# Optimization experiments

Hardware: AMD Instinct MI355X
Metric: run time of the kernel (lower is better)

The kernel has to match this reference:

```python
import jax, jax.numpy as jnp
import numpy as np

BETA = 0.5
TAU_L = 0.1
TAU_H = 0.1
TOP_K = 2


def setup_inputs() -> dict:
    key = jax.random.key(0)
    ks = jax.random.split(key, 6)
    B, S, H, F, E, NH = 1, 2048, 1024, 3584, 8, 16
    hidden_states = jax.random.normal(ks[0], (B, S, H), dtype=jnp.float32)
    self_attn_weights = jax.random.uniform(ks[1], (B, NH, S, S), dtype=jnp.float32)
    gate_w = jax.random.normal(ks[2], (E, H), dtype=jnp.float32) * 0.02
    w1 = jax.random.normal(ks[3], (E, F, H), dtype=jnp.float32) * 0.02
    w2 = jax.random.normal(ks[4], (E, H, F), dtype=jnp.float32) * 0.02
    w3 = jax.random.normal(ks[5], (E, F, H), dtype=jnp.float32) * 0.02
    return {"hidden_states": hidden_states, "self_attn_weights": self_attn_weights,
            "gate_w": gate_w, "w1": w1, "w2": w2, "w3": w3}


def reference(hidden_states, self_attn_weights, gate_w, w1, w2, w3):
    B, S, H = hidden_states.shape
    E = gate_w.shape[0]
    x = hidden_states.reshape(-1, H)          # [T, H], T = B*S
    T = x.shape[0]

    router_logits = x @ gate_w.T              # [T, E]
    rw_full = jax.nn.softmax(router_logits.astype(jnp.float32), axis=-1)
    rw, sel = jax.lax.top_k(rw_full, TOP_K)   # [T, 2]

    # --- dynamic pruning branch (loss_index < block_range) ---
    mask_top1 = rw[:, 1] < BETA * rw[:, 0]
    new_routing = jnp.ones_like(rw)
    new_routing = new_routing.at[:, 1].set(jnp.where(mask_top1, 0.0, 1.0))

    # sequence_length > 1: attention-based token pruning (assumes B == 1)
    mean_tensor = jnp.mean(jnp.squeeze(self_attn_weights), axis=0)  # [S, S]
    column = mean_tensor.shape[1]
    real_number = jnp.arange(column, 0, -1, dtype=jnp.float32)
    attention_scores = jnp.sum(mean_tensor, axis=1) / real_number   # [S]
    l1_norm = jnp.sum(jnp.abs(x), axis=1)                           # [T]
    attention_scores = attention_scores * l1_norm

    n_low = int(TAU_L * T)
    n_high = int(TAU_H * T)
    _, low_idx = jax.lax.top_k(-attention_scores, n_low)   # smallest
    _, high_idx = jax.lax.top_k(attention_scores, n_high)  # largest
    mask_all = jnp.zeros((T,), dtype=bool).at[low_idx].set(True)
    keep_all = jnp.zeros((T,), dtype=bool).at[high_idx].set(True)
    new_routing = jnp.where(mask_all[:, None], 0.0, new_routing)
    new_routing = jnp.where(keep_all[:, None], 1.0, new_routing)

    rw = rw * new_routing
    denom = jnp.sum(rw, axis=-1, keepdims=True)
    rw = rw / jnp.where(denom > 0, denom, 1.0)  # fully-masked tokens -> 0 output
    rw = rw.astype(x.dtype)

    # combine weights per (token, expert); dispatch mask == new_routing
    cw = jnp.sum(rw[:, :, None] * jax.nn.one_hot(sel, E, dtype=rw.dtype), axis=1)  # [T, E]

    # dense reference for the gather-expert-scatter loop (SwiGLU experts)
    h = jnp.einsum('th,efh->tef', x, w1)      # [T, E, F]
    g = jnp.einsum('th,efh->tef', x, w3)
    a = jax.nn.silu(h) * g
    y = jnp.einsum('tef,ehf->teh', a, w2)     # [T, E, H]
    out = jnp.einsum('te,teh->th', cw, y)     # [T, H]

    return out.reshape(B, S, H), router_logits
```

## Files before the change

kernel.cpp:

```cpp
#include <hip/hip_runtime.h>
#include <hip/hip_bf16.h>
#include <math.h>

#define NTOK 2048
#define HDIM 1024
#define NEXP 8
#define FDIM 3584
#define NHEADS 16
#define NLOW 204
#define NHIGH 204
#define BK 64
#define KSPLIT 4
#define KCH (FDIM / KSPLIT)

typedef __bf16 bf16x8 __attribute__((ext_vector_type(8)));
typedef float f32x4 __attribute__((ext_vector_type(4)));

__device__ __forceinline__ void gload16(__hip_bfloat16* lds, const __hip_bfloat16* g)
{
    __builtin_amdgcn_global_load_lds(
        (const __attribute__((address_space(1))) unsigned int*)g,
        (__attribute__((address_space(3))) unsigned int*)lds, 16, 0, 0);
}

__device__ __forceinline__ void cvt8(const float* __restrict__ s,
                                     __hip_bfloat16* __restrict__ d)
{
    float4 a = *(const float4*)s;
    float4 b = *(const float4*)(s + 4);
    bf16x8 v;
    v[0] = (__bf16)a.x; v[1] = (__bf16)a.y; v[2] = (__bf16)a.z; v[3] = (__bf16)a.w;
    v[4] = (__bf16)b.x; v[5] = (__bf16)b.y; v[6] = (__bf16)b.z; v[7] = (__bf16)b.w;
    *(bf16x8*)d = v;
}

#define NZ   (NTOK * HDIM / 4)
#define NX   (NTOK * HDIM / 8)
#define NWT  (NEXP * FDIM * HDIM / 8)
__global__ __launch_bounds__(256) void k_prep(
    const float* __restrict__ x, const float* __restrict__ w1,
    const float* __restrict__ w3, float4* __restrict__ outz,
    __hip_bfloat16* __restrict__ xb, __hip_bfloat16* __restrict__ wb1,
    __hip_bfloat16* __restrict__ wb3)
{
    size_t gid = (size_t)blockIdx.x * 256 + threadIdx.x;
    size_t stride = (size_t)gridDim.x * 256;
    size_t total = (size_t)NZ + NX + 2 * (size_t)NWT;
    for (size_t i = gid; i < total; i += stride) {
        if (i < NZ) {
            outz[i] = make_float4(0.f, 0.f, 0.f, 0.f);
        } else if (i < (size_t)NZ + NX) {
            size_t j = (i - NZ) * 8;
            cvt8(x + j, xb + j);
        } else if (i < (size_t)NZ + NX + NWT) {
            size_t j = (i - NZ - NX) * 8;
            cvt8(w1 + j, wb1 + j);
        } else {
            size_t j = (i - NZ - NX - NWT) * 8;
            cvt8(w3 + j, wb3 + j);
        }
    }
}

__global__ __launch_bounds__(256) void k_router(
    const float* __restrict__ x, const float* __restrict__ gw,
    float* __restrict__ logits, float* __restrict__ l1,
    int* __restrict__ sel0, int* __restrict__ sel1,
    float* __restrict__ rw0, float* __restrict__ rw1)
{
    __shared__ float sgw[NEXP * HDIM];
    int tid = threadIdx.x;
    for (int i = tid; i < NEXP * HDIM; i += 256) sgw[i] = gw[i];
    __syncthreads();
    int wv = tid >> 6, lane = tid & 63;
    int t = blockIdx.x * 4 + wv;
    const float* xr = x + (size_t)t * HDIM;
    float acc[NEXP];
#pragma unroll
    for (int e = 0; e < NEXP; ++e) acc[e] = 0.f;
    float al1 = 0.f;
    for (int h = lane; h < HDIM; h += 64) {
        float xv = xr[h];
        al1 += fabsf(xv);
#pragma unroll
        for (int e = 0; e < NEXP; ++e) acc[e] += xv * sgw[e * HDIM + h];
    }
#pragma unroll
    for (int off = 32; off > 0; off >>= 1) {
#pragma unroll
        for (int e = 0; e < NEXP; ++e) acc[e] += __shfl_xor(acc[e], off);
        al1 += __shfl_xor(al1, off);
    }
    if (lane < NEXP) logits[t * NEXP + lane] = acc[lane];
    if (lane == 0) {
        l1[t] = al1;
        float m = acc[0];
#pragma unroll
        for (int e = 1; e < NEXP; ++e) m = fmaxf(m, acc[e]);
        float p[NEXP], s = 0.f;
#pragma unroll
        for (int e = 0; e < NEXP; ++e) { p[e] = expf(acc[e] - m); s += p[e]; }
        float inv = 1.f / s;
        float b0 = -1.f, b1 = -1.f; int i0 = 0, i1 = 0;
#pragma unroll
        for (int e = 0; e < NEXP; ++e) {
            float r = p[e] * inv;
            if (r > b0) { b1 = b0; i1 = i0; b0 = r; i0 = e; }
            else if (r > b1) { b1 = r; i1 = e; }
        }
        sel0[t] = i0; sel1[t] = i1; rw0[t] = b0; rw1[t] = b1;
    }
}

__global__ __launch_bounds__(256) void k_attn(
    const float* __restrict__ attn, const float* __restrict__ l1,
    float* __restrict__ scores)
{
    int i = blockIdx.x, tid = threadIdx.x;
    float acc = 0.f;
    for (int h = 0; h < NHEADS; ++h) {
        const float4* p = (const float4*)(attn + ((size_t)h * NTOK + i) * NTOK);
        for (int j = tid; j < NTOK / 4; j += 256) {
            float4 v = p[j];
            acc += v.x + v.y + v.z + v.w;
        }
    }
    __shared__ float red[256];
    red[tid] = acc; __syncthreads();
    for (int s = 128; s > 0; s >>= 1) {
        if (tid < s) red[tid] += red[tid + s];
        __syncthreads();
    }
    if (tid == 0) scores[i] = red[0] / (16.f * (float)(NTOK - i)) * l1[i];
}

__global__ __launch_bounds__(256) void k_rank(
    const float* __restrict__ scores, const float* __restrict__ rw0,
    const float* __restrict__ rw1, float* __restrict__ w0f, float* __restrict__ w1f)
{
    __shared__ float s[NTOK];
    int tid = threadIdx.x;
    for (int i = tid; i < NTOK; i += 256) s[i] = scores[i];
    __syncthreads();
    int t = blockIdx.x * 256 + tid;
    float st = s[t];
    int cl = 0, ch = 0;
    for (int j = 0; j < NTOK; ++j) {
        float sj = s[j];
        int tie = (sj == st) && (j < t);
        cl += (sj < st) || tie;
        ch += (sj > st) || tie;
    }
    bool in_low = cl < NLOW, keep = ch < NHIGH;
    float a = rw0[t], b = rw1[t];
    float n0 = 1.f, n1 = (b < 0.5f * a) ? 0.f : 1.f;
    if (in_low) { n0 = 0.f; n1 = 0.f; }
    if (keep)   { n0 = 1.f; n1 = 1.f; }
    a *= n0; b *= n1;
    float d = a + b;
    if (d > 0.f) { a /= d; b /= d; }
    w0f[t] = a; w1f[t] = b;
}

__global__ __launch_bounds__(512) void k_build(
    const int* __restrict__ sel0, const int* __restrict__ sel1,
    const float* __restrict__ w0f, const float* __restrict__ w1f,
    int* __restrict__ tok, float* __restrict__ wgt,
    int* __restrict__ counts, int* __restrict__ offs)
{
    int tid = threadIdx.x;
    int e = tid >> 6, lane = tid & 63;
    unsigned long long below = (1ull << lane) - 1ull;
    int base = 0;
    for (int r = 0; r < NTOK / 64; ++r) {
        int t = r * 64 + lane;
        bool f0 = (sel0[t] == e) && (w0f[t] > 0.f);
        unsigned long long m0 = __ballot(f0);
        if (f0) {
            int pos = base + __popcll(m0 & below);
            tok[e * NTOK + pos] = t; wgt[e * NTOK + pos] = w0f[t];
        }
        base += __popcll(m0);
        bool f1 = (sel1[t] == e) && (w1f[t] > 0.f);
        unsigned long long m1 = __ballot(f1);
        if (f1) {
            int pos = base + __popcll(m1 & below);
            tok[e * NTOK + pos] = t; wgt[e * NTOK + pos] = w1f[t];
        }
        base += __popcll(m1);
    }
    if (lane == 0) counts[e] = base;
    __syncthreads();
    if (tid == 0) {
        int o = 0;
        for (int i = 0; i < NEXP; ++i) { offs[i] = o; o += counts[i]; }
    }
}

__global__ __launch_bounds__(256, 3) void k_ffn1(
    const __hip_bfloat16* __restrict__ xb, const __hip_bfloat16* __restrict__ wb1,
    const __hip_bfloat16* __restrict__ wb3,
    const float* __restrict__ w2, __hip_bfloat16* __restrict__ wb2,
    const int* __restrict__ tok, const float* __restrict__ wgt,
    const int* __restrict__ counts, const int* __restrict__ offs,
    __hip_bfloat16* __restrict__ act)
{
    int tid = threadIdx.x;
    if (blockIdx.z == 0) {
        size_t gid = ((size_t)(blockIdx.y * gridDim.x + blockIdx.x) * 256 + tid);
        size_t stride = (size_t)gridDim.x * gridDim.y * 256;
        for (size_t i = gid; i < (size_t)NWT; i += stride)
            cvt8(w2 + i * 8, wb2 + i * 8);
        return;
    }
    int e = blockIdx.z - 1;
    int cnt = counts[e];
    int m0 = blockIdx.y * 128;
    if (m0 >= cnt) return;
    int f0 = blockIdx.x * 64;
    __shared__ __align__(16) __hip_bfloat16 sX[128 * BK];
    __shared__ __align__(16) __hip_bfloat16 sW1[64 * BK];
    __shared__ __align__(16) __hip_bfloat16 sW3[64 * BK];
    __shared__ int sTok[128];
    __shared__ float sWgt[128];
    if (tid < 128) {
        int row = m0 + tid;
        int rr = (row < cnt) ? row : (cnt - 1);
        sTok[tid] = tok[e * NTOK + rr];
        sWgt[tid] = (row < cnt) ? wgt[e * NTOK + row] : 0.f;
    }
    __syncthreads();

    int wv = tid >> 6, lane = tid & 63;
    int lr = lane >> 3;
    int sw8 = (((lane & 7) ^ lr) << 3);

    const __hip_bfloat16* gx[4];
    __hip_bfloat16* lx[4];
#pragma unroll
    for (int j = 0; j < 4; ++j) {
        int c = 4 * wv + j;
        gx[j] = xb + (size_t)sTok[8 * c + lr] * HDIM + sw8;
        lx[j] = sX + c * 512;
    }
    const __hip_bfloat16* gw1[2]; const __hip_bfloat16* gw3[2];
    __hip_bfloat16* lw1[2]; __hip_bfloat16* lw3[2];
#pragma unroll
    for (int j = 0; j < 2; ++j) {
        int c = 2 * wv + j;
        gw1[j] = wb1 + ((size_t)e * FDIM + f0 + 8 * c + lr) * HDIM + sw8;
        gw3[j] = wb3 + ((size_t)e * FDIM + f0 + 8 * c + lr) * HDIM + sw8;
        lw1[j] = sW1 + c * 512;
        lw3[j] = sW3 + c * 512;
    }

    int colx = lane & 15;
    int swz = (colx & 7) << 4;
    int kb0 = (lane >> 4) * 16;
    f32x4 acc1[2][4] = {}, acc3[2][4] = {};

    for (int k0 = 0; k0 < HDIM; k0 += BK) {
#pragma unroll
        for (int j = 0; j < 4; ++j) gload16(lx[j], gx[j] + k0);
#pragma unroll
        for (int j = 0; j < 2; ++j) {
            gload16(lw1[j], gw1[j] + k0);
            gload16(lw3[j], gw3[j] + k0);
        }
        __syncthreads();
#pragma unroll
        for (int ks = 0; ks < 2; ++ks) {
            int off = ((kb0 + ks * 64) ^ swz) >> 1;
            bf16x8 a_[2];
#pragma unroll
            for (int m = 0; m < 2; ++m) {
                int row = 32 * wv + m * 16 + colx;
                a_[m] = *(const bf16x8*)&sX[(row << 6) + off];
            }
#pragma unroll
            for (int f = 0; f < 4; ++f) {
                int row = f * 16 + colx;
                bf16x8 b1 = *(const bf16x8*)&sW1[(row << 6) + off];
                bf16x8 b3 = *(const bf16x8*)&sW3[(row << 6) + off];
#pragma unroll
                for (int m = 0; m < 2; ++m) {
                    acc1[m][f] = __builtin_amdgcn_mfma_f32_16x16x32_bf16(a_[m], b1, acc1[m][f], 0, 0, 0);
                    acc3[m][f] = __builtin_amdgcn_mfma_f32_16x16x32_bf16(a_[m], b3, acc3[m][f], 0, 0, 0);
                }
            }
        }
        __syncthreads();
    }
    int soff = offs[e];
    int lane4 = (lane >> 4) * 4;
#pragma unroll
    for (int m = 0; m < 2; ++m) {
        int rbase = 32 * wv + m * 16 + lane4;
#pragma unroll
        for (int q = 0; q < 4; ++q) {
            int rloc = rbase + q;
            if (m0 + rloc < cnt) {
                float wgtv = sWgt[rloc];
#pragma unroll
                for (int f = 0; f < 4; ++f) {
                    float hv = acc1[m][f][q], gv = acc3[m][f][q];
                    float av = hv / (1.f + expf(-hv)) * gv * wgtv;
                    act[(size_t)(soff + m0 + rloc) * FDIM + f0 + f * 16 + colx] =
                        (__hip_bfloat16)av;
                }
            }
        }
    }
}

__global__ __launch_bounds__(256, 4) void k_ffn2(
    const __hip_bfloat16* __restrict__ act, const __hip_bfloat16* __restrict__ wb2,
    const int* __restrict__ tok, const int* __restrict__ counts,
    const int* __restrict__ offs, float* __restrict__ out)
{
    int z = blockIdx.z;
    int e = z >> 2;
    int kbase = (z & 3) * KCH;
    int cnt = counts[e];
    int m0 = blockIdx.y * 128;
    if (m0 >= cnt) return;
    int h0 = blockIdx.x * 64;
    int tid = threadIdx.x;
    __shared__ __align__(16) __hip_bfloat16 sA[128 * BK];
    __shared__ __align__(16) __hip_bfloat16 sB[64 * BK];
    __shared__ int sTok[128];
    if (tid < 128) {
        int row = m0 + tid;
        sTok[tid] = (row < cnt) ? tok[e * NTOK + row] : 0;
    }
    __syncthreads();
    int soff = offs[e];
    int wv = tid >> 6, lane = tid & 63;
    int lr = lane >> 3;
    int sw8 = (((lane & 7) ^ lr) << 3);

    const __hip_bfloat16* ga[4];
    __hip_bfloat16* la[4];
#pragma unroll
    for (int j = 0; j < 4; ++j) {
        int c = 4 * wv + j;
        int trow = 8 * c + lr;
        int arow = (m0 + trow < cnt) ? (m0 + trow) : (cnt - 1);
        ga[j] = act + (size_t)(soff + arow) * FDIM + kbase + sw8;
        la[j] = sA + c * 512;
    }
    const __hip_bfloat16* gb[2];
    __hip_bfloat16* lb[2];
#pragma unroll
    for (int j = 0; j < 2; ++j) {
        int c = 2 * wv + j;
        gb[j] = wb2 + ((size_t)e * HDIM + h0 + 8 * c + lr) * FDIM + kbase + sw8;
        lb[j] = sB + c * 512;
    }

    int colx = lane & 15;
    int swz = (colx & 7) << 4;
    int kb0 = (lane >> 4) * 16;
    f32x4 acc[2][4] = {};

    for (int k0 = 0; k0 < KCH; k0 += BK) {
#pragma unroll
        for (int j = 0; j < 4; ++j) gload16(la[j], ga[j] + k0);
#pragma unroll
        for (int j = 0; j < 2; ++j) gload16(lb[j], gb[j] + k0);
        __syncthreads();
#pragma unroll
        for (int ks = 0; ks < 2; ++ks) {
            int off = ((kb0 + ks * 64) ^ swz) >> 1;
            bf16x8 a_[2];
#pragma unroll
            for (int m = 0; m < 2; ++m) {
                int row = 32 * wv + m * 16 + colx;
                a_[m] = *(const bf16x8*)&sA[(row << 6) + off];
            }
#pragma unroll
            for (int f = 0; f < 4; ++f) {
                int row = f * 16 + colx;
                bf16x8 b = *(const bf16x8*)&sB[(row << 6) + off];
#pragma unroll
                for (int m = 0; m < 2; ++m)
                    acc[m][f] = __builtin_amdgcn_mfma_f32_16x16x32_bf16(a_[m], b, acc[m][f], 0, 0, 0);
            }
        }
        __syncthreads();
    }
    int lane4 = (lane >> 4) * 4;
#pragma unroll
    for (int m = 0; m < 2; ++m) {
        int rbase = 32 * wv + m * 16 + lane4;
#pragma unroll
        for (int q = 0; q < 4; ++q) {
            int rloc = rbase + q;
            if (m0 + rloc < cnt) {
                int t = sTok[rloc];
#pragma unroll
                for (int f = 0; f < 4; ++f)
                    atomicAdd(&out[(size_t)t * HDIM + h0 + f * 16 + colx], acc[m][f][q]);
            }
        }
    }
}

extern "C" void kernel_launch(void* const* d_in, const int* in_sizes, int n_in,
                              void* d_out, int out_size, void* d_ws, size_t ws_size,
                              hipStream_t stream)
{
    const float* x    = (const float*)d_in[0];
    const float* attn = (const float*)d_in[1];
    const float* gw   = (const float*)d_in[2];
    const float* w1   = (const float*)d_in[3];
    const float* w2   = (const float*)d_in[4];
    const float* w3   = (const float*)d_in[5];
    float* out = (float*)d_out;
    float* logits = out + (size_t)NTOK * HDIM;

    char* ws = (char*)d_ws;
    float* l1     = (float*)(ws + 0);
    float* scores = (float*)(ws + 8192);
    int*   sel0   = (int*)(ws + 16384);
    int*   sel1   = (int*)(ws + 24576);
    float* rw0    = (float*)(ws + 32768);
    float* rw1    = (float*)(ws + 40960);
    float* w0f    = (float*)(ws + 49152);
    float* w1f    = (float*)(ws + 57344);
    int*   counts = (int*)(ws + 65536);
    int*   offs   = (int*)(ws + 65600);
    int*   tok    = (int*)(ws + 73728);
    float* wgt    = (float*)(ws + 143360);
    __hip_bfloat16* act = (__hip_bfloat16*)(ws + 1048576);
    __hip_bfloat16* xb  = (__hip_bfloat16*)(ws + 33554432);
    __hip_bfloat16* wb1 = (__hip_bfloat16*)(ws + 67108864);
    __hip_bfloat16* wb3 = (__hip_bfloat16*)(ws + 134217728);
    __hip_bfloat16* wb2 = (__hip_bfloat16*)(ws + 201326592);

    k_prep<<<4096, 256, 0, stream>>>(x, w1, w3, (float4*)out, xb, wb1, wb3);
    k_router<<<NTOK / 4, 256, 0, stream>>>(x, gw, logits, l1, sel0, sel1, rw0, rw1);
    k_attn<<<NTOK, 256, 0, stream>>>(attn, l1, scores);
    k_rank<<<NTOK / 256, 256, 0, stream>>>(scores, rw0, rw1, w0f, w1f);
    k_build<<<1, 512, 0, stream>>>(sel0, sel1, w0f, w1f, tok, wgt, counts, offs);
    k_ffn1<<<dim3(FDIM / 64, NTOK / 128, NEXP + 1), 256, 0, stream>>>(
        xb, wb1, wb3, w2, wb2, tok, wgt, counts, offs, act);
    k_ffn2<<<dim3(HDIM / 64, NTOK / 128, NEXP * KSPLIT), 256, 0, stream>>>(
        act, wb2, tok, counts, offs, out);
}
```

Before: 407.2 us.

## Fuse attention row-sum into prep kernel and raise ffn2 split-K to 8

Merges the attention-score reduction into the front conversion kernel as extra blocks, so the two memory-bound passes share one launch and can overlap. The l1 scaling moves into the ranking kernel. It also doubles the K-split for the second expert GEMM to increase block-level parallelism, at the cost of more atomic accumulations into the output.

```diff
diff --git a/kernel.cpp b/kernel.cpp
--- a/kernel.cpp
+++ b/kernel.cpp
@@ -10,7 +10,7 @@
 #define NLOW 204
 #define NHIGH 204
 #define BK 64
-#define KSPLIT 4
+#define KSPLIT 8
 #define KCH (FDIM / KSPLIT)
 
 typedef __bf16 bf16x8 __attribute__((ext_vector_type(8)));
@@ -37,14 +37,36 @@
 #define NZ   (NTOK * HDIM / 4)
 #define NX   (NTOK * HDIM / 8)
 #define NWT  (NEXP * FDIM * HDIM / 8)
-__global__ __launch_bounds__(256) void k_prep(
-    const float* __restrict__ x, const float* __restrict__ w1,
-    const float* __restrict__ w3, float4* __restrict__ outz,
+
+__global__ __launch_bounds__(256) void k_front(
+    const float* __restrict__ attn, const float* __restrict__ x,
+    const float* __restrict__ w1, const float* __restrict__ w3,
+    float* __restrict__ rawsum, float4* __restrict__ outz,
     __hip_bfloat16* __restrict__ xb, __hip_bfloat16* __restrict__ wb1,
     __hip_bfloat16* __restrict__ wb3)
 {
-    size_t gid = (size_t)blockIdx.x * 256 + threadIdx.x;
-    size_t stride = (size_t)gridDim.x * 256;
+    __shared__ float red[256];
+    int bid = blockIdx.x, tid = threadIdx.x;
+    if (bid < NTOK) {
+        int i = bid;
+        float acc = 0.f;
+        for (int h = 0; h < NHEADS; ++h) {
+            const float4* p = (const float4*)(attn + ((size_t)h * NTOK + i) * NTOK);
+            for (int j = tid; j < NTOK / 4; j += 256) {
+                float4 v = p[j];
+                acc += v.x + v.y + v.z + v.w;
+            }
+        }
+        red[tid] = acc; __syncthreads();
+        for (int s = 128; s > 0; s >>= 1) {
+            if (tid < s) red[tid] += red[tid + s];
+            __syncthreads();
+        }
+        if (tid == 0) rawsum[i] = red[0];
+        return;
+    }
+    size_t gid = (size_t)(bid - NTOK) * 256 + tid;
+    size_t stride = (size_t)(gridDim.x - NTOK) * 256;
     size_t total = (size_t)NZ + NX + 2 * (size_t)NWT;
     for (size_t i = gid; i < total; i += stride) {
         if (i < NZ) {
@@ -112,35 +134,15 @@
     }
 }
 
-__global__ __launch_bounds__(256) void k_attn(
-    const float* __restrict__ attn, const float* __restrict__ l1,
-    float* __restrict__ scores)
-{
-    int i = blockIdx.x, tid = threadIdx.x;
-    float acc = 0.f;
-    for (int h = 0; h < NHEADS; ++h) {
-        const float4* p = (const float4*)(attn + ((size_t)h * NTOK + i) * NTOK);
-        for (int j = tid; j < NTOK / 4; j += 256) {
-            float4 v = p[j];
-            acc += v.x + v.y + v.z + v.w;
-        }
-    }
-    __shared__ float red[256];
-    red[tid] = acc; __syncthreads();
-    for (int s = 128; s > 0; s >>= 1) {
-        if (tid < s) red[tid] += red[tid + s];
-        __syncthreads();
-    }
-    if (tid == 0) scores[i] = red[0] / (16.f * (float)(NTOK - i)) * l1[i];
-}
-
 __global__ __launch_bounds__(256) void k_rank(
-    const float* __restrict__ scores, const float* __restrict__ rw0,
-    const float* __restrict__ rw1, float* __restrict__ w0f, float* __restrict__ w1f)
+    const float* __restrict__ rawsum, const float* __restrict__ l1,
+    const float* __restrict__ rw0, const float* __restrict__ rw1,
+    float* __restrict__ w0f, float* __restrict__ w1f)
 {
     __shared__ float s[NTOK];
     int tid = threadIdx.x;
-    for (int i = tid; i < NTOK; i += 256) s[i] = scores[i];
+    for (int i = tid; i < NTOK; i += 256)
+        s[i] = rawsum[i] / (16.f * (float)(NTOK - i)) * l1[i];
     __syncthreads();
     int t = blockIdx.x * 256 + tid;
     float st = s[t];
@@ -319,8 +321,8 @@
     const int* __restrict__ offs, float* __restrict__ out)
 {
     int z = blockIdx.z;
-    int e = z >> 2;
-    int kbase = (z & 3) * KCH;
+    int e = z >> 3;
+    int kbase = (z & 7) * KCH;
     int cnt = counts[e];
     int m0 = blockIdx.y * 128;
     if (m0 >= cnt) return;
@@ -421,7 +423,7 @@
 
     char* ws = (char*)d_ws;
     float* l1     = (float*)(ws + 0);
-    float* scores = (float*)(ws + 8192);
+    float* rawsum = (float*)(ws + 8192);
     int*   sel0   = (int*)(ws + 16384);
     int*   sel1   = (int*)(ws + 24576);
     float* rw0    = (float*)(ws + 32768);
@@ -438,10 +440,10 @@
     __hip_bfloat16* wb3 = (__hip_bfloat16*)(ws + 134217728);
     __hip_bfloat16* wb2 = (__hip_bfloat16*)(ws + 201326592);
 
-    k_prep<<<4096, 256, 0, stream>>>(x, w1, w3, (float4*)out, xb, wb1, wb3);
+    k_front<<<4096, 256, 0, stream>>>(attn, x, w1, w3, rawsum, (float4*)out,
+                                      xb, wb1, wb3);
     k_router<<<NTOK / 4, 256, 0, stream>>>(x, gw, logits, l1, sel0, sel1, rw0, rw1);
-    k_attn<<<NTOK, 256, 0, stream>>>(attn, l1, scores);
-    k_rank<<<NTOK / 256, 256, 0, stream>>>(scores, rw0, rw1, w0f, w1f);
+    k_rank<<<NTOK / 256, 256, 0, stream>>>(rawsum, l1, rw0, rw1, w0f, w1f);
     k_build<<<1, 512, 0, stream>>>(sel0, sel1, w0f, w1f, tok, wgt, counts, offs);
     k_ffn1<<<dim3(FDIM / 64, NTOK / 128, NEXP + 1), 256, 0, stream>>>(
         xb, wb1, wb3, w2, wb2, tok, wgt, counts, offs, act);
```

Result: slower. 433.6 us (+6.5%).

## Fuse fp32-to-bf16 conversion of w1/w3 into register-prefetched double-buffered FFN1 GEMM

Applied to the files above, without the earlier changes.

The separate pre-pass that converted w1 and w3 from fp32 to bf16 in global memory is removed. k_ffn1 now loads fp32 weights directly, converts them in registers, and stores them into double-buffered padded LDS tiles, prefetching the next K slice during the MFMAs. The F tile grows to 128 with a 64x64 per-wave output and BK drops to 32. This avoids writing and re-reading bf16 weight copies, but each token tile re-reads fp32 weights (twice the bytes per load), and the larger accumulator set raises register pressure, so occupancy is lowered to 2.

```diff
diff --git a/kernel.cpp b/kernel.cpp
--- a/kernel.cpp
+++ b/kernel.cpp
@@ -9,7 +9,9 @@
 #define NHEADS 16
 #define NLOW 204
 #define NHIGH 204
-#define BK 64
+#define BK1 32
+#define LDST 40
+#define BK2 64
 #define KSPLIT 4
 #define KCH (FDIM / KSPLIT)
 
@@ -34,30 +36,43 @@
     *(bf16x8*)d = v;
 }
 
+struct F16v { float4 a, b, c, d; };
+__device__ __forceinline__ F16v ld16(const float* __restrict__ p)
+{
+    F16v v;
+    v.a = *(const float4*)p;
+    v.b = *(const float4*)(p + 4);
+    v.c = *(const float4*)(p + 8);
+    v.d = *(const float4*)(p + 12);
+    return v;
+}
+__device__ __forceinline__ void st16(__hip_bfloat16* dst, const F16v& v)
+{
+    bf16x8 lo, hi;
+    lo[0] = (__bf16)v.a.x; lo[1] = (__bf16)v.a.y; lo[2] = (__bf16)v.a.z; lo[3] = (__bf16)v.a.w;
+    lo[4] = (__bf16)v.b.x; lo[5] = (__bf16)v.b.y; lo[6] = (__bf16)v.b.z; lo[7] = (__bf16)v.b.w;
+    hi[0] = (__bf16)v.c.x; hi[1] = (__bf16)v.c.y; hi[2] = (__bf16)v.c.z; hi[3] = (__bf16)v.c.w;
+    hi[4] = (__bf16)v.d.x; hi[5] = (__bf16)v.d.y; hi[6] = (__bf16)v.d.z; hi[7] = (__bf16)v.d.w;
+    *(bf16x8*)dst = lo;
+    *(bf16x8*)(dst + 8) = hi;
+}
+
 #define NZ   (NTOK * HDIM / 4)
 #define NX   (NTOK * HDIM / 8)
 #define NWT  (NEXP * FDIM * HDIM / 8)
 __global__ __launch_bounds__(256) void k_prep(
-    const float* __restrict__ x, const float* __restrict__ w1,
-    const float* __restrict__ w3, float4* __restrict__ outz,
-    __hip_bfloat16* __restrict__ xb, __hip_bfloat16* __restrict__ wb1,
-    __hip_bfloat16* __restrict__ wb3)
+    const float* __restrict__ x, float4* __restrict__ outz,
+    __hip_bfloat16* __restrict__ xb)
 {
     size_t gid = (size_t)blockIdx.x * 256 + threadIdx.x;
     size_t stride = (size_t)gridDim.x * 256;
-    size_t total = (size_t)NZ + NX + 2 * (size_t)NWT;
+    size_t total = (size_t)NZ + NX;
     for (size_t i = gid; i < total; i += stride) {
         if (i < NZ) {
             outz[i] = make_float4(0.f, 0.f, 0.f, 0.f);
-        } else if (i < (size_t)NZ + NX) {
+        } else {
             size_t j = (i - NZ) * 8;
             cvt8(x + j, xb + j);
-        } else if (i < (size_t)NZ + NX + NWT) {
-            size_t j = (i - NZ - NX) * 8;
-            cvt8(w1 + j, wb1 + j);
-        } else {
-            size_t j = (i - NZ - NX - NWT) * 8;
-            cvt8(w3 + j, wb3 + j);
         }
     }
 }
@@ -197,9 +212,9 @@
     }
 }
 
-__global__ __launch_bounds__(256, 3) void k_ffn1(
-    const __hip_bfloat16* __restrict__ xb, const __hip_bfloat16* __restrict__ wb1,
-    const __hip_bfloat16* __restrict__ wb3,
+__global__ __launch_bounds__(256, 2) void k_ffn1(
+    const __hip_bfloat16* __restrict__ xb, const float* __restrict__ w1,
+    const float* __restrict__ w3,
     const float* __restrict__ w2, __hip_bfloat16* __restrict__ wb2,
     const int* __restrict__ tok, const float* __restrict__ wgt,
     const int* __restrict__ counts, const int* __restrict__ offs,
@@ -217,10 +232,10 @@
     int cnt = counts[e];
     int m0 = blockIdx.y * 128;
     if (m0 >= cnt) return;
-    int f0 = blockIdx.x * 64;
-    __shared__ __align__(16) __hip_bfloat16 sX[128 * BK];
-    __shared__ __align__(16) __hip_bfloat16 sW1[64 * BK];
-    __shared__ __align__(16) __hip_bfloat16 sW3[64 * BK];
+    int f0 = blockIdx.x * 128;
+    __shared__ __align__(16) __hip_bfloat16 sX[2][128 * LDST];
+    __shared__ __align__(16) __hip_bfloat16 sW1[2][128 * LDST];
+    __shared__ __align__(16) __hip_bfloat16 sW3[2][128 * LDST];
     __shared__ int sTok[128];
     __shared__ float sWgt[128];
     if (tid < 128) {
@@ -231,81 +246,75 @@
     }
     __syncthreads();
 
+    int r = tid >> 1, c16 = (tid & 1) * 16;
+    const __hip_bfloat16* xp = xb + (size_t)sTok[r] * HDIM + c16;
+    const float* w1p = w1 + ((size_t)e * FDIM + f0 + r) * HDIM + c16;
+    const float* w3p = w3 + ((size_t)e * FDIM + f0 + r) * HDIM + c16;
+    int sidx = r * LDST + c16;
+
+    {
+        bf16x8 x0 = *(const bf16x8*)xp, x1 = *(const bf16x8*)(xp + 8);
+        F16v w0 = ld16(w1p), g0 = ld16(w3p);
+        *(bf16x8*)&sX[0][sidx] = x0;
+        *(bf16x8*)&sX[0][sidx + 8] = x1;
+        st16(&sW1[0][sidx], w0);
+        st16(&sW3[0][sidx], g0);
+    }
+    __syncthreads();
+
     int wv = tid >> 6, lane = tid & 63;
-    int lr = lane >> 3;
-    int sw8 = (((lane & 7) ^ lr) << 3);
-
-    const __hip_bfloat16* gx[4];
-    __hip_bfloat16* lx[4];
-#pragma unroll
-    for (int j = 0; j < 4; ++j) {
-        int c = 4 * wv + j;
-        gx[j] = xb + (size_t)sTok[8 * c + lr] * HDIM + sw8;
-        lx[j] = sX + c * 512;
-    }
-    const __hip_bfloat16* gw1[2]; const __hip_bfloat16* gw3[2];
-    __hip_bfloat16* lw1[2]; __hip_bfloat16* lw3[2];
-#pragma unroll
-    for (int j = 0; j < 2; ++j) {
-        int c = 2 * wv + j;
-        gw1[j] = wb1 + ((size_t)e * FDIM + f0 + 8 * c + lr) * HDIM + sw8;
-        gw3[j] = wb3 + ((size_t)e * FDIM + f0 + 8 * c + lr) * HDIM + sw8;
-        lw1[j] = sW1 + c * 512;
-        lw3[j] = sW3 + c * 512;
-    }
-
-    int colx = lane & 15;
-    int swz = (colx & 7) << 4;
-    int kb0 = (lane >> 4) * 16;
-    f32x4 acc1[2][4] = {}, acc3[2][4] = {};
-
-    for (int k0 = 0; k0 < HDIM; k0 += BK) {
-#pragma unroll
-        for (int j = 0; j < 4; ++j) gload16(lx[j], gx[j] + k0);
-#pragma unroll
-        for (int j = 0; j < 2; ++j) {
-            gload16(lw1[j], gw1[j] + k0);
-            gload16(lw3[j], gw3[j] + k0);
+    int wm = (wv >> 1) * 64, wf = (wv & 1) * 64;
+    int col = lane & 15, kfrag = (lane >> 4) * 8;
+    f32x4 acc1[4][4] = {}, acc3[4][4] = {};
+    int cur = 0;
+    for (int k0 = 0; k0 < HDIM; k0 += BK1) {
+        bool more = (k0 + BK1) < HDIM;
+        bf16x8 xn0, xn1; F16v wn, gn;
+        if (more) {
+            xn0 = *(const bf16x8*)(xp + k0 + BK1);
+            xn1 = *(const bf16x8*)(xp + k0 + BK1 + 8);
+            wn = ld16(w1p + k0 + BK1);
+            gn = ld16(w3p + k0 + BK1);
+        }
+        bf16x8 af[4], b1f[4], b3f[4];
+#pragma unroll
+        for (int m = 0; m < 4; ++m)
+            af[m] = *(const bf16x8*)&sX[cur][(wm + m * 16 + col) * LDST + kfrag];
+#pragma unroll
+        for (int f = 0; f < 4; ++f) {
+            b1f[f] = *(const bf16x8*)&sW1[cur][(wf + f * 16 + col) * LDST + kfrag];
+            b3f[f] = *(const bf16x8*)&sW3[cur][(wf + f * 16 + col) * LDST + kfrag];
+        }
+#pragma unroll
+        for (int m = 0; m < 4; ++m)
+#pragma unroll
+            for (int f = 0; f < 4; ++f) {
+                acc1[m][f] = __builtin_amdgcn_mfma_f32_16x16x32_bf16(af[m], b1f[f], acc1[m][f], 0, 0, 0);
+                acc3[m][f] = __builtin_amdgcn_mfma_f32_16x16x32_bf16(af[m], b3f[f], acc3[m][f], 0, 0, 0);
+            }
+        if (more) {
+            *(bf16x8*)&sX[cur ^ 1][sidx] = xn0;
+            *(bf16x8*)&sX[cur ^ 1][sidx + 8] = xn1;
+            st16(&sW1[cur ^ 1][sidx], wn);
+            st16(&sW3[cur ^ 1][sidx], gn);
         }
         __syncthreads();
-#pragma unroll
-        for (int ks = 0; ks < 2; ++ks) {
-            int off = ((kb0 + ks * 64) ^ swz) >> 1;
-            bf16x8 a_[2];
-#pragma unroll
-            for (int m = 0; m < 2; ++m) {
-                int row = 32 * wv + m * 16 + colx;
-                a_[m] = *(const bf16x8*)&sX[(row << 6) + off];
-            }
-#pragma unroll
-            for (int f = 0; f < 4; ++f) {
-                int row = f * 16 + colx;
-                bf16x8 b1 = *(const bf16x8*)&sW1[(row << 6) + off];
-                bf16x8 b3 = *(const bf16x8*)&sW3[(row << 6) + off];
-#pragma unroll
-                for (int m = 0; m < 2; ++m) {
-                    acc1[m][f] = __builtin_amdgcn_mfma_f32_16x16x32_bf16(a_[m], b1, acc1[m][f], 0, 0, 0);
-                    acc3[m][f] = __builtin_amdgcn_mfma_f32_16x16x32_bf16(a_[m], b3, acc3[m][f], 0, 0, 0);
-                }
-            }
-        }
-        __syncthreads();
+        cur ^= 1;
     }
     int soff = offs[e];
-    int lane4 = (lane >> 4) * 4;
-#pragma unroll
-    for (int m = 0; m < 2; ++m) {
-        int rbase = 32 * wv + m * 16 + lane4;
+#pragma unroll
+    for (int m = 0; m < 4; ++m) {
+        int mb = wm + m * 16 + (lane >> 4) * 4;
 #pragma unroll
         for (int q = 0; q < 4; ++q) {
-            int rloc = rbase + q;
+            int rloc = mb + q;
             if (m0 + rloc < cnt) {
                 float wgtv = sWgt[rloc];
 #pragma unroll
                 for (int f = 0; f < 4; ++f) {
                     float hv = acc1[m][f][q], gv = acc3[m][f][q];
                     float av = hv / (1.f + expf(-hv)) * gv * wgtv;
-                    act[(size_t)(soff + m0 + rloc) * FDIM + f0 + f * 16 + colx] =
+                    act[(size_t)(soff + m0 + rloc) * FDIM + f0 + wf + f * 16 + col] =
                         (__hip_bfloat16)av;
                 }
             }
@@ -326,8 +335,8 @@
     if (m0 >= cnt) return;
     int h0 = blockIdx.x * 64;
     int tid = threadIdx.x;
-    __shared__ __align__(16) __hip_bfloat16 sA[128 * BK];
-    __shared__ __align__(16) __hip_bfloat16 sB[64 * BK];
+    __shared__ __align__(16) __hip_bfloat16 sA[128 * BK2];
+    __shared__ __align__(16) __hip_bfloat16 sB[64 * BK2];
     __shared__ int sTok[128];
     if (tid < 128) {
         int row = m0 + tid;
@@ -363,7 +372,7 @@
     int kb0 = (lane >> 4) * 16;
     f32x4 acc[2][4] = {};
 
-    for (int k0 = 0; k0 < KCH; k0 += BK) {
+    for (int k0 = 0; k0 < KCH; k0 += BK2) {
 #pragma unroll
         for (int j = 0; j < 4; ++j) gload16(la[j], ga[j] + k0);
 #pragma unroll
@@ -434,17 +443,15 @@
     float* wgt    = (float*)(ws + 143360);
     __hip_bfloat16* act = (__hip_bfloat16*)(ws + 1048576);
     __hip_bfloat16* xb  = (__hip_bfloat16*)(ws + 33554432);
-    __hip_bfloat16* wb1 = (__hip_bfloat16*)(ws + 67108864);
-    __hip_bfloat16* wb3 = (__hip_bfloat16*)(ws + 134217728);
-    __hip_bfloat16* wb2 = (__hip_bfloat16*)(ws + 201326592);
-
-    k_prep<<<4096, 256, 0, stream>>>(x, w1, w3, (float4*)out, xb, wb1, wb3);
+    __hip_bfloat16* wb2 = (__hip_bfloat16*)(ws + 67108864);
+
+    k_prep<<<1024, 256, 0, stream>>>(x, (float4*)out, xb);
     k_router<<<NTOK / 4, 256, 0, stream>>>(x, gw, logits, l1, sel0, sel1, rw0, rw1);
     k_attn<<<NTOK, 256, 0, stream>>>(attn, l1, scores);
     k_rank<<<NTOK / 256, 256, 0, stream>>>(scores, rw0, rw1, w0f, w1f);
     k_build<<<1, 512, 0, stream>>>(sel0, sel1, w0f, w1f, tok, wgt, counts, offs);
-    k_ffn1<<<dim3(FDIM / 64, NTOK / 128, NEXP + 1), 256, 0, stream>>>(
-        xb, wb1, wb3, w2, wb2, tok, wgt, counts, offs, act);
+    k_ffn1<<<dim3(FDIM / 128, NTOK / 128, NEXP + 1), 256, 0, stream>>>(
+        xb, w1, w3, w2, wb2, tok, wgt, counts, offs, act);
     k_ffn2<<<dim3(HDIM / 64, NTOK / 128, NEXP * KSPLIT), 256, 0, stream>>>(
         act, wb2, tok, counts, offs, out);
 }
```

Result: no change. 400.8 us (median of 3 runs) (-1.6%).
